# Kernel optimization log

Measured on AMD Instinct MI355X. Metric: run time of the kernel, lower is better.

Reference implementation:

```python
import jax, jax.numpy as jnp
import numpy as np

N_NODES = 100000
N_EDGES = 640000
D_IN = 128
D_OUT = 128


def setup_inputs() -> dict:
    key = jax.random.key(0)
    k1, k2, k3, k4, k5 = jax.random.split(key, 5)
    feats = jax.random.normal(k1, (N_NODES, D_IN), dtype=jnp.float32)
    src = jax.random.randint(k2, (N_EDGES,), 0, N_NODES, dtype=jnp.int32)
    dst = jax.random.randint(k3, (N_EDGES,), 0, N_NODES, dtype=jnp.int32)
    # Xavier-normal-ish init (gain for relu = sqrt(2))
    std = float(np.sqrt(2.0) * np.sqrt(2.0 / (D_IN + D_OUT)))
    linear_skip_weight = jax.random.normal(k4, (D_OUT, D_IN), dtype=jnp.float32) * std
    linear_msg_weight = jax.random.normal(k5, (D_OUT, D_IN), dtype=jnp.float32) * std
    linear_skip_bias = jnp.zeros((D_OUT,), dtype=jnp.float32)
    linear_msg_bias = jnp.zeros((D_OUT,), dtype=jnp.float32)
    return {
        "feats": feats,
        "src": src,
        "dst": dst,
        "linear_skip_weight": linear_skip_weight,
        "linear_skip_bias": linear_skip_bias,
        "linear_msg_weight": linear_msg_weight,
        "linear_msg_bias": linear_msg_bias,
    }


def reference(feats, src, dst, linear_skip_weight, linear_skip_bias,
              linear_msg_weight, linear_msg_bias):
    n = feats.shape[0]
    # degree from scatter-add of edge weights (ones) at source rows
    deg = jax.ops.segment_sum(jnp.ones_like(src, dtype=feats.dtype), src,
                              num_segments=n)
    deg_inv_sqrt = jnp.where(deg > 0, jax.lax.rsqrt(jnp.maximum(deg, 1.0)) * (deg > 0), 0.0)
    deg_inv_sqrt = jnp.where(deg > 0, deg ** -0.5, 0.0)
    # normalize source features, gather along edges, scatter-sum to dst
    feat_src = feats * deg_inv_sqrt[:, None]           # [N, D_IN]
    msgs = feat_src[src]                               # [E, D_IN]
    rst = jax.ops.segment_sum(msgs, dst, num_segments=n)  # [N, D_IN]
    rst = rst * deg_inv_sqrt[:, None]
    rst_ = rst @ linear_msg_weight.T + linear_msg_bias
    skip_x = feats @ linear_skip_weight.T + linear_skip_bias
    return rst_ + skip_x
```

## Files before the change

kernel.cpp:

```cpp
#include <hip/hip_runtime.h>

#define N_NODES 100000
#define N_EDGES 640000
#define D 128
#define NB ((N_NODES + 1023) / 1024)
#define BKT_C 16
#define OVF_CAP 32768

typedef short v8s __attribute__((ext_vector_type(8)));
typedef float v4f __attribute__((ext_vector_type(4)));

__device__ __forceinline__ unsigned short f2bf(float x) {
    unsigned int u = __builtin_bit_cast(unsigned int, x);
    u += 0x7fffu + ((u >> 16) & 1u);
    return (unsigned short)(u >> 16);
}
__device__ __forceinline__ float bf2f(unsigned int hi) {
    return __builtin_bit_cast(float, hi << 16);
}

__global__ __launch_bounds__(256) void k_zero(int4* __restrict__ pk4,
                                              int* __restrict__ ovf_cnt) {
    int i = blockIdx.x * blockDim.x + threadIdx.x;
    if (i < N_NODES / 4) pk4[i] = make_int4(0, 0, 0, 0);
    if (i == 0) *ovf_cnt = 0;
}

__global__ __launch_bounds__(256) void k_pre(const float* __restrict__ feats,
                                             const float* __restrict__ Wm,
                                             const float* __restrict__ Ws,
                                             const float* __restrict__ bmsg,
                                             const float* __restrict__ bskip,
                                             const int* __restrict__ src,
                                             const int* __restrict__ dst,
                                             unsigned int* __restrict__ pk,
                                             unsigned short* __restrict__ Bcat,
                                             float* __restrict__ bias,
                                             char* __restrict__ outb,
                                             int* __restrict__ bucket,
                                             int* __restrict__ ovf_cnt,
                                             int2* __restrict__ ovf) {
    int i = blockIdx.x * blockDim.x + threadIdx.x;
    if (i < D * D) {
        int j = i >> 7;
        int k = i & 127;
        Bcat[j * 256 + k]       = f2bf(Wm[i]);
        Bcat[j * 256 + 128 + k] = f2bf(Ws[i]);
    }
    if (i < D) bias[i] = bmsg[i] + bskip[i];
    if (i < N_EDGES) {
        int s = src[i];
        int d = dst[i];
        atomicAdd(&pk[s], 1u);
        unsigned int old = atomicAdd(&pk[d], 0x10000u);
        if (bucket) {
            unsigned int p = old >> 16;
            if (p < BKT_C) {
                bucket[d * BKT_C + (int)p] = s;
            } else {
                int q = atomicAdd(ovf_cnt, 1);
                if (q < OVF_CAP) ovf[q] = make_int2(d, s);
            }
        }
    }
    int g = i * 8;
    int row = g >> 7;
    int col = g & 127;
    if (row < N_NODES) {
        const float4* sp = (const float4*)(feats + g);
        float4 x = sp[0], y = sp[1];
        uint4 p;
        p.x = (unsigned)f2bf(x.x) | ((unsigned)f2bf(x.y) << 16);
        p.y = (unsigned)f2bf(x.z) | ((unsigned)f2bf(x.w) << 16);
        p.z = (unsigned)f2bf(y.x) | ((unsigned)f2bf(y.y) << 16);
        p.w = (unsigned)f2bf(y.z) | ((unsigned)f2bf(y.w) << 16);
        *(uint4*)(outb + (size_t)row * 512 + 256 + col * 2) = p;
    }
}

__global__ __launch_bounds__(256) void k_scan1(const unsigned int* __restrict__ pk,
                                               int* __restrict__ rowptr,
                                               int* __restrict__ bsums) {
    __shared__ int sd[256];
    int t = threadIdx.x;
    int i0 = blockIdx.x * 1024 + t * 4;
    int v[4];
    int s = 0;
#pragma unroll
    for (int q = 0; q < 4; q++) {
        int i = i0 + q;
        v[q] = (i < N_NODES) ? (int)(pk[i] >> 16) : 0;
        s += v[q];
    }
    sd[t] = s;
    __syncthreads();
    for (int off = 1; off < 256; off <<= 1) {
        int y = (t >= off) ? sd[t - off] : 0;
        __syncthreads();
        sd[t] += y;
        __syncthreads();
    }
    int run = sd[t] - s;
    if (t == 255) bsums[blockIdx.x] = sd[255];
#pragma unroll
    for (int q = 0; q < 4; q++) {
        int i = i0 + q;
        if (i < N_NODES) rowptr[i] = run;
        run += v[q];
    }
}

__global__ __launch_bounds__(128) void k_scan2(int* __restrict__ bsums) {
    __shared__ int sd[128];
    int t = threadIdx.x;
    int v = (t < NB) ? bsums[t] : 0;
    sd[t] = v;
    __syncthreads();
    for (int off = 1; off < 128; off <<= 1) {
        int y = (t >= off) ? sd[t - off] : 0;
        __syncthreads();
        sd[t] += y;
        __syncthreads();
    }
    if (t < NB) bsums[t] = sd[t] - v;
}

__global__ __launch_bounds__(256) void k_scan3(const int* __restrict__ bsums,
                                               int* __restrict__ rowptr) {
    int add = bsums[blockIdx.x];
    int i0 = blockIdx.x * 1024 + threadIdx.x * 4;
#pragma unroll
    for (int q = 0; q < 4; q++) {
        int i = i0 + q;
        if (i < N_NODES) rowptr[i] += add;
    }
}

__global__ __launch_bounds__(256) void k_fill(const int* __restrict__ src,
                                              const int* __restrict__ dst,
                                              int* __restrict__ rowptr,
                                              int* __restrict__ csr_src) {
    int e = blockIdx.x * blockDim.x + threadIdx.x;
    if (e < N_EDGES) {
        int p = atomicAdd(&rowptr[dst[e]], 1);
        csr_src[p] = src[e];
    }
}

__device__ __forceinline__ void agg_edge(const char* outb,
                                         const unsigned int* pk,
                                         int s, int sub, float* acc) {
    float sc = rsqrtf((float)(pk[s] & 0xffffu));
    uint4 v = *(const uint4*)(outb + (size_t)s * 512 + 256 + sub * 16);
    acc[0] += bf2f(v.x & 0xffffu) * sc;
    acc[1] += bf2f(v.x >> 16) * sc;
    acc[2] += bf2f(v.y & 0xffffu) * sc;
    acc[3] += bf2f(v.y >> 16) * sc;
    acc[4] += bf2f(v.z & 0xffffu) * sc;
    acc[5] += bf2f(v.z >> 16) * sc;
    acc[6] += bf2f(v.w & 0xffffu) * sc;
    acc[7] += bf2f(v.w >> 16) * sc;
}

__device__ __forceinline__ void agg_finish(char* outb, int wid,
                                           unsigned int pkn, int grp, int sub,
                                           float* acc) {
#pragma unroll
    for (int i = 0; i < 8; i++) {
        acc[i] += __shfl_xor(acc[i], 16);
        acc[i] += __shfl_xor(acc[i], 32);
    }
    if (grp == 0) {
        int dsrc = (int)(pkn & 0xffffu);
        float scn = (dsrc > 0) ? rsqrtf((float)dsrc) : 0.0f;
        uint4 p;
        p.x = (unsigned)f2bf(acc[0] * scn) | ((unsigned)f2bf(acc[1] * scn) << 16);
        p.y = (unsigned)f2bf(acc[2] * scn) | ((unsigned)f2bf(acc[3] * scn) << 16);
        p.z = (unsigned)f2bf(acc[4] * scn) | ((unsigned)f2bf(acc[5] * scn) << 16);
        p.w = (unsigned)f2bf(acc[6] * scn) | ((unsigned)f2bf(acc[7] * scn) << 16);
        *(uint4*)(outb + (size_t)wid * 512 + sub * 16) = p;
    }
}

__global__ __launch_bounds__(256) void k_agg_bkt(char* __restrict__ outb,
                                                 const unsigned int* __restrict__ pk,
                                                 const int* __restrict__ bucket,
                                                 const int* __restrict__ ovf_cnt,
                                                 const int2* __restrict__ ovf) {
    int wid = (int)((blockIdx.x * (unsigned)blockDim.x + threadIdx.x) >> 6);
    int lane = threadIdx.x & 63;
    if (wid >= N_NODES) return;
    int grp = lane >> 4;
    int sub = lane & 15;
    unsigned int pkn = pk[wid];
    int cnt = (int)(pkn >> 16);
    int m = cnt < BKT_C ? cnt : BKT_C;
    const int* bk = bucket + wid * BKT_C;
    float acc[8];
#pragma unroll
    for (int i = 0; i < 8; i++) acc[i] = 0.f;

    for (int base = 0; base < m; base += 4) {
        int e = base + grp;
        if (e < m) agg_edge(outb, pk, bk[e], sub, acc);
    }
    if (cnt > BKT_C) {
        int no = *ovf_cnt;
        if (no > OVF_CAP) no = OVF_CAP;
        for (int i = grp; i < no; i += 4) {
            int2 p = ovf[i];
            if (p.x == wid) agg_edge(outb, pk, p.y, sub, acc);
        }
    }
    agg_finish(outb, wid, pkn, grp, sub, acc);
}

__global__ __launch_bounds__(256) void k_agg_csr(char* __restrict__ outb,
                                                 const unsigned int* __restrict__ pk,
                                                 const int* __restrict__ rowptr,
                                                 const int* __restrict__ csr_src) {
    int wid = (int)((blockIdx.x * (unsigned)blockDim.x + threadIdx.x) >> 6);
    int lane = threadIdx.x & 63;
    if (wid >= N_NODES) return;
    int grp = lane >> 4;
    int sub = lane & 15;
    int start = (wid == 0) ? 0 : rowptr[wid - 1];
    int end = rowptr[wid];
    float acc[8];
#pragma unroll
    for (int i = 0; i < 8; i++) acc[i] = 0.f;
    for (int base = start; base < end; base += 4) {
        int e = base + grp;
        if (e < end) agg_edge(outb, pk, csr_src[e], sub, acc);
    }
    agg_finish(outb, wid, pk[wid], grp, sub, acc);
}

__global__ __launch_bounds__(256) void k_gemm(const unsigned short* __restrict__ Bcat,
                                              const float* __restrict__ bias,
                                              float* __restrict__ outf) {
    __shared__ unsigned short Bl[128][264];
    const char* Ab = (const char*)outf;
    int tid = threadIdx.x;
    int lane = tid & 63;
    int w = tid >> 6;
    int n0 = blockIdx.x * 128;

    for (int i = tid; i < 128 * 32; i += 256) {
        int r = i >> 5, c = i & 31;
        *(uint4*)(&Bl[r][c * 8]) = *(const uint4*)(Bcat + r * 256 + c * 8);
    }
    __syncthreads();

    int q = lane >> 4;
    int lr = lane & 15;

    int r0 = n0 + w * 32 + lr;      if (r0 > N_NODES - 1) r0 = N_NODES - 1;
    int r1 = n0 + w * 32 + 16 + lr; if (r1 > N_NODES - 1) r1 = N_NODES - 1;
    const char* a0p = Ab + (size_t)r0 * 512 + q * 16;
    const char* a1p = Ab + (size_t)r1 * 512 + q * 16;

    v4f acc[2][8];
#pragma unroll
    for (int mt = 0; mt < 2; mt++)
#pragma unroll
        for (int t = 0; t < 8; t++) acc[mt][t] = (v4f){0.f, 0.f, 0.f, 0.f};

#pragma unroll
    for (int kk = 0; kk < 8; kk++) {
        v8s a0 = *(const v8s*)(a0p + kk * 64);
        v8s a1 = *(const v8s*)(a1p + kk * 64);
#pragma unroll
        for (int t = 0; t < 8; t++) {
            v8s b = *(const v8s*)(&Bl[t * 16 + lr][kk * 32 + q * 8]);
            acc[0][t] = __builtin_amdgcn_mfma_f32_16x16x32_bf16(a0, b, acc[0][t], 0, 0, 0);
            acc[1][t] = __builtin_amdgcn_mfma_f32_16x16x32_bf16(a1, b, acc[1][t], 0, 0, 0);
        }
    }

#pragma unroll
    for (int t = 0; t < 8; t++) {
        float bv = bias[t * 16 + lr];
#pragma unroll
        for (int mt = 0; mt < 2; mt++) {
            int rowb = n0 + w * 32 + mt * 16 + q * 4;
#pragma unroll
            for (int r = 0; r < 4; r++) {
                int row = rowb + r;
                if (row < N_NODES)
                    outf[(size_t)row * 128 + t * 16 + lr] = acc[mt][t][r] + bv;
            }
        }
    }
}

extern "C" void kernel_launch(void* const* d_in, const int* in_sizes, int n_in,
                              void* d_out, int out_size, void* d_ws, size_t ws_size,
                              hipStream_t stream) {
    const float* feats = (const float*)d_in[0];
    const int*   src   = (const int*)d_in[1];
    const int*   dst   = (const int*)d_in[2];
    const float* Wskip = (const float*)d_in[3];
    const float* bskip = (const float*)d_in[4];
    const float* Wmsg  = (const float*)d_in[5];
    const float* bmsg  = (const float*)d_in[6];

    char* w = (char*)d_ws;

    bool pathA = ws_size >= (size_t)7128320;

    if (pathA) {
        unsigned int*   pk      = (unsigned int*)w;
        int*            ovf_cnt = (int*)(w + 400000);
        unsigned short* Bcat    = (unsigned short*)(w + 400128);
        float*          bias    = (float*)(w + 465664);
        int*            bucket  = (int*)(w + 466176);
        int2*           ovf     = (int2*)(w + 6866176);

        hipLaunchKernelGGL(k_zero, dim3((N_NODES / 4 + 255) / 256), dim3(256), 0,
                           stream, (int4*)pk, ovf_cnt);
        hipLaunchKernelGGL(k_pre, dim3((N_NODES * (D / 8) + 255) / 256), dim3(256),
                           0, stream, feats, Wmsg, Wskip, bmsg, bskip, src, dst, pk,
                           Bcat, bias, (char*)d_out, bucket, ovf_cnt, ovf);
        hipLaunchKernelGGL(k_agg_bkt, dim3((N_NODES * 64 + 255) / 256), dim3(256), 0,
                           stream, (char*)d_out, pk, bucket, ovf_cnt, ovf);
        hipLaunchKernelGGL(k_gemm, dim3((N_NODES + 127) / 128), dim3(256), 0, stream,
                           Bcat, bias, (float*)d_out);
    } else {
        unsigned int*   pk      = (unsigned int*)w;
        int*            rowptr  = (int*)(w + 400000);
        int*            bsums   = (int*)(w + 800128);
        unsigned short* Bcat    = (unsigned short*)(w + 800640);
        float*          bias    = (float*)(w + 866176);
        int*            csr_src = (int*)(w + 866688);

        hipLaunchKernelGGL(k_zero, dim3((N_NODES / 4 + 255) / 256), dim3(256), 0,
                           stream, (int4*)pk, (int*)(w + 400000) );
        hipLaunchKernelGGL(k_pre, dim3((N_NODES * (D / 8) + 255) / 256), dim3(256),
                           0, stream, feats, Wmsg, Wskip, bmsg, bskip, src, dst, pk,
                           Bcat, bias, (char*)d_out, (int*)nullptr, (int*)nullptr,
                           (int2*)nullptr);
        hipLaunchKernelGGL(k_scan1, dim3(NB), dim3(256), 0, stream, pk, rowptr,
                           bsums);
        hipLaunchKernelGGL(k_scan2, dim3(1), dim3(128), 0, stream, bsums);
        hipLaunchKernelGGL(k_scan3, dim3(NB), dim3(256), 0, stream, bsums, rowptr);
        hipLaunchKernelGGL(k_fill, dim3((N_EDGES + 255) / 256), dim3(256), 0, stream,
                           src, dst, rowptr, csr_src);
        hipLaunchKernelGGL(k_agg_csr, dim3((N_NODES * 64 + 255) / 256), dim3(256), 0,
                           stream, (char*)d_out, pk, rowptr, csr_src);
        hipLaunchKernelGGL(k_gemm, dim3((N_NODES + 127) / 128), dim3(256), 0, stream,
                           Bcat, bias, (float*)d_out);
    }
}
```

Before: 236.8 us.

## Unroll bucket aggregation into batched loads, hoist feature loads, memset instead of zero kernel

```diff
diff --git a/kernel.cpp b/kernel.cpp
--- a/kernel.cpp
+++ b/kernel.cpp
@@ -17,13 +17,6 @@
 }
 __device__ __forceinline__ float bf2f(unsigned int hi) {
     return __builtin_bit_cast(float, hi << 16);
-}
-
-__global__ __launch_bounds__(256) void k_zero(int4* __restrict__ pk4,
-                                              int* __restrict__ ovf_cnt) {
-    int i = blockIdx.x * blockDim.x + threadIdx.x;
-    if (i < N_NODES / 4) pk4[i] = make_int4(0, 0, 0, 0);
-    if (i == 0) *ovf_cnt = 0;
 }
 
 __global__ __launch_bounds__(256) void k_pre(const float* __restrict__ feats,
@@ -41,6 +34,18 @@
                                              int* __restrict__ ovf_cnt,
                                              int2* __restrict__ ovf) {
     int i = blockIdx.x * blockDim.x + threadIdx.x;
+
+    int g = i * 8;
+    int row = g >> 7;
+    int col = g & 127;
+    float4 x, y;
+    bool do_pack = row < N_NODES;
+    if (do_pack) {
+        const float4* sp = (const float4*)(feats + g);
+        x = sp[0];
+        y = sp[1];
+    }
+
     if (i < D * D) {
         int j = i >> 7;
         int k = i & 127;
@@ -48,6 +53,7 @@
         Bcat[j * 256 + 128 + k] = f2bf(Ws[i]);
     }
     if (i < D) bias[i] = bmsg[i] + bskip[i];
+
     if (i < N_EDGES) {
         int s = src[i];
         int d = dst[i];
@@ -63,12 +69,8 @@
             }
         }
     }
-    int g = i * 8;
-    int row = g >> 7;
-    int col = g & 127;
-    if (row < N_NODES) {
-        const float4* sp = (const float4*)(feats + g);
-        float4 x = sp[0], y = sp[1];
+
+    if (do_pack) {
         uint4 p;
         p.x = (unsigned)f2bf(x.x) | ((unsigned)f2bf(x.y) << 16);
         p.y = (unsigned)f2bf(x.z) | ((unsigned)f2bf(x.w) << 16);
@@ -152,6 +154,17 @@
                                          int s, int sub, float* acc) {
     float sc = rsqrtf((float)(pk[s] & 0xffffu));
     uint4 v = *(const uint4*)(outb + (size_t)s * 512 + 256 + sub * 16);
+    acc[0] += bf2f(v.x & 0xffffu) * sc;
+    acc[1] += bf2f(v.x >> 16) * sc;
+    acc[2] += bf2f(v.y & 0xffffu) * sc;
+    acc[3] += bf2f(v.y >> 16) * sc;
+    acc[4] += bf2f(v.z & 0xffffu) * sc;
+    acc[5] += bf2f(v.z >> 16) * sc;
+    acc[6] += bf2f(v.w & 0xffffu) * sc;
+    acc[7] += bf2f(v.w >> 16) * sc;
+}
+
+__device__ __forceinline__ void agg_acc(uint4 v, float sc, float* acc) {
     acc[0] += bf2f(v.x & 0xffffu) * sc;
     acc[1] += bf2f(v.x >> 16) * sc;
     acc[2] += bf2f(v.y & 0xffffu) * sc;
@@ -196,14 +209,38 @@
     int cnt = (int)(pkn >> 16);
     int m = cnt < BKT_C ? cnt : BKT_C;
     const int* bk = bucket + wid * BKT_C;
+
+    int4 bq = *(const int4*)(bk + grp * 4);
+    int e0 = grp * 4;
+
+    bool a0 = e0 < m, a1 = e0 + 1 < m, a2 = e0 + 2 < m, a3 = e0 + 3 < m;
+    int sA = a0 ? bq.x : 0; float gA = a0 ? 1.0f : 0.0f;
+    int sB = a1 ? bq.y : 0; float gB = a1 ? 1.0f : 0.0f;
+    int sC = a2 ? bq.z : 0; float gC = a2 ? 1.0f : 0.0f;
+    int sD = a3 ? bq.w : 0; float gD = a3 ? 1.0f : 0.0f;
+
+    unsigned int pA = pk[sA];
+    unsigned int pB = pk[sB];
+    unsigned int pC = pk[sC];
+    unsigned int pD = pk[sD];
+    uint4 vA = *(const uint4*)(outb + (size_t)sA * 512 + 256 + sub * 16);
+    uint4 vB = *(const uint4*)(outb + (size_t)sB * 512 + 256 + sub * 16);
+    uint4 vC = *(const uint4*)(outb + (size_t)sC * 512 + 256 + sub * 16);
+    uint4 vD = *(const uint4*)(outb + (size_t)sD * 512 + 256 + sub * 16);
+
+    float scA = gA * rsqrtf(fmaxf((float)(pA & 0xffffu), 1.0f));
+    float scB = gB * rsqrtf(fmaxf((float)(pB & 0xffffu), 1.0f));
+    float scC = gC * rsqrtf(fmaxf((float)(pC & 0xffffu), 1.0f));
+    float scD = gD * rsqrtf(fmaxf((float)(pD & 0xffffu), 1.0f));
+
     float acc[8];
 #pragma unroll
     for (int i = 0; i < 8; i++) acc[i] = 0.f;
-
-    for (int base = 0; base < m; base += 4) {
-        int e = base + grp;
-        if (e < m) agg_edge(outb, pk, bk[e], sub, acc);
-    }
+    agg_acc(vA, scA, acc);
+    agg_acc(vB, scB, acc);
+    agg_acc(vC, scC, acc);
+    agg_acc(vD, scD, acc);
+
     if (cnt > BKT_C) {
         int no = *ovf_cnt;
         if (no > OVF_CAP) no = OVF_CAP;
@@ -311,14 +348,13 @@
 
     if (pathA) {
         unsigned int*   pk      = (unsigned int*)w;
-        int*            ovf_cnt = (int*)(w + 400000);
         unsigned short* Bcat    = (unsigned short*)(w + 400128);
         float*          bias    = (float*)(w + 465664);
         int*            bucket  = (int*)(w + 466176);
+        int*            ovf_cnt = (int*)(w + 400000);
         int2*           ovf     = (int2*)(w + 6866176);
 
-        hipLaunchKernelGGL(k_zero, dim3((N_NODES / 4 + 255) / 256), dim3(256), 0,
-                           stream, (int4*)pk, ovf_cnt);
+        hipMemsetAsync(w, 0, 400128, stream);
         hipLaunchKernelGGL(k_pre, dim3((N_NODES * (D / 8) + 255) / 256), dim3(256),
                            0, stream, feats, Wmsg, Wskip, bmsg, bskip, src, dst, pk,
                            Bcat, bias, (char*)d_out, bucket, ovf_cnt, ovf);
@@ -334,8 +370,7 @@
         float*          bias    = (float*)(w + 866176);
         int*            csr_src = (int*)(w + 866688);
 
-        hipLaunchKernelGGL(k_zero, dim3((N_NODES / 4 + 255) / 256), dim3(256), 0,
-                           stream, (int4*)pk, (int*)(w + 400000) );
+        hipMemsetAsync(w, 0, 400000, stream);
         hipLaunchKernelGGL(k_pre, dim3((N_NODES * (D / 8) + 255) / 256), dim3(256),
                            0, stream, feats, Wmsg, Wskip, bmsg, bskip, src, dst, pk,
                            Bcat, bias, (char*)d_out, (int*)nullptr, (int*)nullptr,
```

New measurement: 240.3 us. No clear change (+1.5%).
